# Kernel tuning notes

Measured on AMD Instinct MI355X. Metric: run time of the kernel, lower is better.

The kernel has to match this reference:

```python
import jax, jax.numpy as jnp
from jax import lax
import numpy as np

DN = ('NCHW', 'OIHW', 'NCHW')

def conv(x, w, b, stride=1, groups=1):
    y = lax.conv_general_dilated(x, w, (stride, stride), 'SAME',
                                 feature_group_count=groups, dimension_numbers=DN)
    return y + b[None, :, None, None]

def sep_conv(x, dw, pw, pb):
    # depthwise 3x3 -> pointwise 1x1 -> ReLU (BN is frozen at identity)
    y = lax.conv_general_dilated(x, dw, (1, 1), 'SAME',
                                 feature_group_count=x.shape[1], dimension_numbers=DN)
    return jax.nn.relu(conv(y, pw, pb))

def up2(x):
    return jnp.repeat(jnp.repeat(x, 2, axis=2), 2, axis=3)

def down2(x):
    return lax.reduce_window(x, -jnp.inf, lax.max, (1, 1, 2, 2), (1, 1, 2, 2), 'VALID')

def fuse(w, *xs):
    # fast normalized fusion
    w = jax.nn.relu(w)
    w = w / (jnp.sum(w) + 1e-4)
    out = w[0] * xs[0]
    for i in range(1, len(xs)):
        out = out + w[i] * xs[i]
    return out

def bifpn_layer(ps, dw, pw, pb, fw2, fw3):
    p3, p4, p5, p6, p7 = ps
    p6t = sep_conv(fuse(fw2[0], p6, up2(p7)),  dw[0], pw[0], pb[0])
    p5t = sep_conv(fuse(fw2[1], p5, up2(p6t)), dw[1], pw[1], pb[1])
    p4t = sep_conv(fuse(fw2[2], p4, up2(p5t)), dw[2], pw[2], pb[2])
    p3o = sep_conv(fuse(fw2[3], p3, up2(p4t)), dw[3], pw[3], pb[3])
    p4o = sep_conv(fuse(fw3[0], p4, p4t, down2(p3o)), dw[4], pw[4], pb[4])
    p5o = sep_conv(fuse(fw3[1], p5, p5t, down2(p4o)), dw[5], pw[5], pb[5])
    p6o = sep_conv(fuse(fw3[2], p6, p6t, down2(p5o)), dw[6], pw[6], pb[6])
    p7o = sep_conv(fuse(fw2[4], p7, down2(p6o)),      dw[7], pw[7], pb[7])
    return [p3o, p4o, p5o, p6o, p7o]

def make_anchors(img_size):
    # RetinaNet-style anchors: pyramid levels 3..7, 3 scales x 3 ratios
    ratios = np.array([0.5, 1.0, 2.0])
    scales = 2.0 ** (np.arange(3) / 3.0)
    boxes_all = []
    for lvl in range(3, 8):
        stride = 2 ** lvl
        size = 2 ** (lvl + 2)
        fs = img_size // stride
        ws = (size * scales[None, :] / np.sqrt(ratios)[:, None]).reshape(-1)  # [9]
        hs = (size * scales[None, :] * np.sqrt(ratios)[:, None]).reshape(-1)
        ctr = (np.arange(fs) + 0.5) * stride
        gy, gx = np.meshgrid(ctr, ctr, indexing='ij')
        centers = np.stack([gx, gy], -1).reshape(-1, 1, 2)      # [HW,1,2] (x,y)
        wh = np.stack([ws, hs], -1)[None]                       # [1,9,2]
        boxes = np.concatenate([centers - wh / 2, centers + wh / 2], -1).reshape(-1, 4)
        boxes_all.append(boxes)
    return jnp.asarray(np.concatenate(boxes_all, 0), jnp.float32)

def run_head(p, tw, tb, ow, ob, out_ch):
    x = p
    for i in range(tw.shape[0]):
        x = jax.nn.relu(conv(x, tw[i], tb[i]))
    y = conv(x, ow, ob)                                  # [B, 9*out_ch, H, W]
    B, _, H, W = y.shape
    return y.transpose(0, 2, 3, 1).reshape(B, H * W * 9, out_ch)

def setup_inputs() -> dict:
    key = jax.random.key(0)
    ks = iter(jax.random.split(key, 64))
    B, W, NC, ST, D = 4, 88, 90, 3, 4
    chans = [40, 80, 112, 192, 320]
    hw = [64, 32, 16, 8, 4]
    inp = {}
    for i, (c, h) in enumerate(zip(chans, hw)):
        inp[f'c{i+3}'] = jax.random.normal(next(ks), (B, c, h, h), jnp.float32)
        inp[f'lat_w{i+3}'] = jax.random.normal(next(ks), (W, c, 1, 1), jnp.float32) * 0.05
        inp[f'lat_b{i+3}'] = jnp.zeros((W,), jnp.float32)
    inp['bif_dw'] = jax.random.normal(next(ks), (ST, 8, W, 1, 3, 3), jnp.float32) * 0.1
    inp['bif_pw'] = jax.random.normal(next(ks), (ST, 8, W, W, 1, 1), jnp.float32) * 0.05
    inp['bif_pb'] = jnp.zeros((ST, 8, W), jnp.float32)
    inp['bif_fw2'] = jnp.ones((ST, 5, 2), jnp.float32)
    inp['bif_fw3'] = jnp.ones((ST, 3, 3), jnp.float32)
    inp['reg_tw'] = jax.random.normal(next(ks), (D, W, W, 3, 3), jnp.float32) * 0.03
    inp['reg_tb'] = jnp.zeros((D, W), jnp.float32)
    inp['reg_ow'] = jax.random.normal(next(ks), (36, W, 3, 3), jnp.float32) * 0.01
    inp['reg_ob'] = jnp.zeros((36,), jnp.float32)
    inp['cls_tw'] = jax.random.normal(next(ks), (D, W, W, 3, 3), jnp.float32) * 0.03
    inp['cls_tb'] = jnp.zeros((D, W), jnp.float32)
    inp['cls_ow'] = jax.random.normal(next(ks), (9 * NC, W, 3, 3), jnp.float32) * 0.01
    inp['cls_ob'] = jnp.full((9 * NC,), -np.log((1.0 - 0.01) / 0.01), jnp.float32)
    inp['img_size'] = 512
    return inp

def reference(c3, c4, c5, c6, c7,
              lat_w3, lat_b3, lat_w4, lat_b4, lat_w5, lat_b5,
              lat_w6, lat_b6, lat_w7, lat_b7,
              bif_dw, bif_pw, bif_pb, bif_fw2, bif_fw3,
              reg_tw, reg_tb, reg_ow, reg_ob,
              cls_tw, cls_tb, cls_ow, cls_ob,
              img_size):
    num_classes = cls_ow.shape[0] // 9
    ps = [conv(c3, lat_w3, lat_b3), conv(c4, lat_w4, lat_b4), conv(c5, lat_w5, lat_b5),
          conv(c6, lat_w6, lat_b6), conv(c7, lat_w7, lat_b7)]
    for s in range(bif_dw.shape[0]):
        ps = bifpn_layer(ps, bif_dw[s], bif_pw[s], bif_pb[s], bif_fw2[s], bif_fw3[s])
    regression = jnp.concatenate([run_head(p, reg_tw, reg_tb, reg_ow, reg_ob, 4) for p in ps], axis=1)
    classification = jnp.concatenate(
        [jax.nn.sigmoid(run_head(p, cls_tw, cls_tb, cls_ow, cls_ob, num_classes)) for p in ps], axis=1)
    anchors = make_anchors(int(img_size))
    return classification, regression, anchors
```

## Files before the change

kernel.cpp:

```cpp
#include <hip/hip_runtime.h>
#include <math.h>

#define TPB 256
static inline int cdiv(int a, int b) { return (a + b - 1) / b; }

typedef __attribute__((ext_vector_type(8))) short short8;
typedef __attribute__((ext_vector_type(4))) float floatx4;

__device__ __forceinline__ float bf2f(ushort u) {
    union { unsigned int u; float f; } v; v.u = ((unsigned int)u) << 16; return v.f;
}
__device__ __forceinline__ ushort f2bf(float f) {
    union { float f; unsigned int u; } v; v.f = f;
    unsigned int r = (v.u + 0x7FFFu + ((v.u >> 16) & 1u)) >> 16;
    return (ushort)r;
}

#define CONC_ROWS 21824
__device__ __forceinline__ void lvl_of(int row, int& lvl, int& base) {
    lvl = 0; base = 0;
    if (row >= 16384) { lvl = 1; base = 16384; }
    if (row >= 20480) { lvl = 2; base = 20480; }
    if (row >= 21504) { lvl = 3; base = 21504; }
    if (row >= 21760) { lvl = 4; base = 21760; }
}
__constant__ int LOFFc[5] = {0, 36864, 46080, 48384, 48960};

#define BSLAB 9216

__device__ __forceinline__ void gld_lds16(const ushort* g, ushort* l) {
    __builtin_amdgcn_global_load_lds(
        (const __attribute__((address_space(1))) unsigned int*)g,
        (__attribute__((address_space(3))) unsigned int*)l, 16, 0, 0);
}

__global__ void pack3_k(const float* __restrict__ w, ushort* __restrict__ Bp,
                        int Ntot, int CO, int total) {
    int idx = blockIdx.x * blockDim.x + threadIdx.x;
    if (idx >= total) return;
    int j = idx & 7; int t = idx >> 3;
    int n = t % Ntot; t /= Ntot;
    int g = t & 3; t >>= 2;
    int ks = t % 3; int tap = t / 3;
    int ci = ks * 32 + g * 8 + j;
    float v = (ci < 88 && n < CO) ? w[((size_t)n * 88 + ci) * 9 + tap] : 0.f;
    Bp[idx] = f2bf(v);
}

__global__ void pack_cls_k(const float* __restrict__ w, ushort* __restrict__ Bp) {
    int idx = blockIdx.x * blockDim.x + threadIdx.x;
    if (idx >= 746496) return;
    int j = idx & 7; int t = idx >> 3;
    int n = t % 96; t /= 96;
    int g = t & 3; t >>= 2;
    int ks = t % 3; t /= 3;
    int tap = t % 9; int nb = t / 9;
    int ci = ks * 32 + g * 8 + j;
    int co = nb * 96 + n;
    float v = (ci < 88 && co < 810) ? w[((size_t)co * 88 + ci) * 9 + tap] : 0.f;
    Bp[idx] = f2bf(v);
}

__global__ void pack_tw8_k(const float* __restrict__ rw, const float* __restrict__ cw,
                           ushort* __restrict__ Bp) {
    int idx = blockIdx.x * blockDim.x + threadIdx.x;
    if (idx >= 8 * 82944) return;
    int i = idx / 82944; int r = idx - i * 82944;
    const float* w = (i < 4) ? rw + (size_t)i * 69696 : cw + (size_t)(i - 4) * 69696;
    int j = r & 7; int t = r >> 3;
    int n = t % 96; t /= 96;
    int g = t & 3; t >>= 2;
    int ks = t % 3; int tap = t / 3;
    int ci = ks * 32 + g * 8 + j;
    float v = (ci < 88 && n < 88) ? w[((size_t)n * 88 + ci) * 9 + tap] : 0.f;
    Bp[idx] = f2bf(v);
}

__global__ void pack_pw_all_k(const float* __restrict__ pw, ushort* __restrict__ Bp,
                              int total) {
    int idx = blockIdx.x * blockDim.x + threadIdx.x;
    if (idx >= total) return;
    int cid = idx / BSLAB; int r = idx - cid * BSLAB;
    int j = r & 7; int t = r >> 3;
    int n = t % 96; t /= 96;
    int g = t & 3; int ks = t >> 2;
    int ci = ks * 32 + g * 8 + j;
    float v = (ci < 88 && n < 88) ? pw[(size_t)cid * 7744 + n * 88 + ci] : 0.f;
    Bp[idx] = f2bf(v);
}

__global__ void pack_lat_k(const float* __restrict__ w3, const float* __restrict__ w4,
                           const float* __restrict__ w5, const float* __restrict__ w6,
                           const float* __restrict__ w7, ushort* __restrict__ Bp) {
    int idx = blockIdx.x * blockDim.x + threadIdx.x;
    if (idx >= 76800) return;
    int l, off;
    if (idx < 6144)       { l = 0; off = 0; }
    else if (idx < 15360) { l = 1; off = 6144; }
    else if (idx < 27648) { l = 2; off = 15360; }
    else if (idx < 46080) { l = 3; off = 27648; }
    else                  { l = 4; off = 46080; }
    const float* w = l == 0 ? w3 : l == 1 ? w4 : l == 2 ? w5 : l == 3 ? w6 : w7;
    const int cins[5] = {40, 80, 112, 192, 320};
    int Cin = cins[l];
    int r = idx - off;
    int j = r & 7; int t = r >> 3;
    int n = t % 96; t /= 96;
    int g = t & 3; int ks = t >> 2;
    int ci = ks * 32 + g * 8 + j;
    float v = (ci < Cin && n < 88) ? w[(size_t)n * Cin + ci] : 0.f;
    Bp[idx] = f2bf(v);
}

__global__ __launch_bounds__(256)
void lateral_mfma_k(const float* __restrict__ x, const ushort* __restrict__ Bp,
                    const float* __restrict__ bias, ushort* __restrict__ out,
                    int Cin, int KS, int logHH) {
    __shared__ ushort As[64 * 40];
    int tid = threadIdx.x;
    int m0 = blockIdx.x * 64;
    int lane = tid & 63, l15 = lane & 15, g = (lane >> 4) & 3;
    int wave = tid >> 6, wm = wave & 1, wn = wave >> 1;
    floatx4 acc[2][3];
#pragma unroll
    for (int a = 0; a < 2; ++a)
#pragma unroll
        for (int b = 0; b < 3; ++b) acc[a][b] = (floatx4){0.f, 0.f, 0.f, 0.f};
    const short8* Bq = (const short8*)Bp;

    int p = m0 + lane;
    int n = p >> logHH, pp = p & ((1 << logHH) - 1);
    const float* xp = x + (((size_t)n * Cin) << logHH) + pp;

    for (int ks = 0; ks < KS; ++ks) {
        __syncthreads();
#pragma unroll
        for (int it = 0; it < 8; ++it) {
            int ciL = (tid >> 6) + it * 4;
            int ci = ks * 32 + ciL;
            float v = (ci < Cin) ? xp[(size_t)ci << logHH] : 0.f;
            As[lane * 40 + ciL] = f2bf(v);
        }
        __syncthreads();
        short8 a0 = *(const short8*)(&As[(wm * 32 + l15) * 40 + g * 8]);
        short8 a1 = *(const short8*)(&As[(wm * 32 + 16 + l15) * 40 + g * 8]);
        int bbase = (ks * 4 + g) * 96 + wn * 48 + l15;
#pragma unroll
        for (int nf = 0; nf < 3; ++nf) {
            short8 b = Bq[bbase + nf * 16];
            acc[0][nf] = __builtin_amdgcn_mfma_f32_16x16x32_bf16(a0, b, acc[0][nf], 0, 0, 0);
            acc[1][nf] = __builtin_amdgcn_mfma_f32_16x16x32_bf16(a1, b, acc[1][nf], 0, 0, 0);
        }
    }
    float bc[3];
#pragma unroll
    for (int nf = 0; nf < 3; ++nf) {
        int c = wn * 48 + nf * 16 + l15;
        bc[nf] = (c < 88) ? bias[c] : 0.f;
    }
#pragma unroll
    for (int mf = 0; mf < 2; ++mf)
#pragma unroll
        for (int r = 0; r < 4; ++r) {
            int pl = m0 + wm * 32 + mf * 16 + g * 4 + r;
#pragma unroll
            for (int nf = 0; nf < 3; ++nf) {
                int c = wn * 48 + nf * 16 + l15;
                out[(size_t)pl * 96 + c] = f2bf(acc[mf][nf][r] + bc[nf]);
            }
        }
}

template <int MODE>
__global__ __launch_bounds__(256, 2)
void sepconv_k(const ushort* __restrict__ a, const ushort* __restrict__ bsrc,
               const ushort* __restrict__ csrc, const float* __restrict__ fw,
               const float* __restrict__ dww, const ushort* __restrict__ Bp,
               const float* __restrict__ pbias, ushort* __restrict__ out,
               int logW) {
    __shared__ ushort Fs[195 * 104];
    __shared__ ushort Ds[64 * 104];
    __shared__ ushort Dwb[108 * 8];
    int tid = threadIdx.x;
    int W = 1 << logW, HH = W * W, log2HH = 2 * logW;
    int Mlv = 4 * HH;
    int HB = W + 1;
    int RS = 64 + 2 * HB;
    int pl0 = blockIdx.x * 64;
    float w0 = fmaxf(fw[0], 0.f), w1 = fmaxf(fw[1], 0.f);
    float w2 = (MODE == 2) ? fmaxf(fw[2], 0.f) : 0.f;
    float inv = 1.f / (w0 + w1 + w2 + 1e-4f);
    float w0i = w0 * inv, w1i = w1 * inv, w2i = w2 * inv;

    if (tid < 13) *(uint4*)(&Fs[194 * 104 + tid * 8]) = (uint4){0u, 0u, 0u, 0u};
    for (int i = tid; i < 108; i += 256) {
        int cg = i / 9, tap = i - cg * 9;
        ushort tmp[8];
#pragma unroll
        for (int j = 0; j < 8; ++j) {
            int c = cg * 8 + j;
            tmp[j] = (c < 88) ? f2bf(dww[c * 9 + tap]) : (ushort)0;
        }
        *(uint4*)(&Dwb[i * 8]) = *(uint4*)tmp;
    }
    for (int i = tid; i < RS * 12; i += 256) {
        int row = i / 12, cg = i - row * 12;
        int pl = pl0 - HB + row;
        uint4 res = {0u, 0u, 0u, 0u};
        if (pl >= 0 && pl < Mlv) {
            int n = pl >> log2HH, pp = pl & (HH - 1);
            int y = pp >> logW, x = pp & (W - 1);
            uint4 av = *(const uint4*)(a + (size_t)pl * 96 + cg * 8);
            const ushort* au = (const ushort*)&av;
            float f[8];
            if (MODE == 0) {
                int Wh = W >> 1;
                int bp = (n << (log2HH - 2)) + (y >> 1) * Wh + (x >> 1);
                uint4 bv = *(const uint4*)(bsrc + (size_t)bp * 96 + cg * 8);
                const ushort* bu = (const ushort*)&bv;
#pragma unroll
                for (int j = 0; j < 8; ++j)
                    f[j] = w0i * bf2f(au[j]) + w1i * bf2f(bu[j]);
            } else {
                int W2 = W << 1;
                const ushort* q = (MODE == 1 ? bsrc : csrc) +
                    ((size_t)((n << (log2HH + 2)) + (2 * y) * W2 + 2 * x)) * 96 + cg * 8;
                uint4 q0 = *(const uint4*)(q);
                uint4 q1 = *(const uint4*)(q + 96);
                uint4 q2 = *(const uint4*)(q + (size_t)W2 * 96);
                uint4 q3 = *(const uint4*)(q + (size_t)W2 * 96 + 96);
                const ushort* u0 = (const ushort*)&q0; const ushort* u1 = (const ushort*)&q1;
                const ushort* u2 = (const ushort*)&q2; const ushort* u3 = (const ushort*)&q3;
                if (MODE == 1) {
#pragma unroll
                    for (int j = 0; j < 8; ++j) {
                        float m = fmaxf(fmaxf(bf2f(u0[j]), bf2f(u1[j])),
                                        fmaxf(bf2f(u2[j]), bf2f(u3[j])));
                        f[j] = w0i * bf2f(au[j]) + w1i * m;
                    }
                } else {
                    uint4 b2v = *(const uint4*)(bsrc + (size_t)pl * 96 + cg * 8);
                    const ushort* b2u = (const ushort*)&b2v;
#pragma unroll
                    for (int j = 0; j < 8; ++j) {
                        float m = fmaxf(fmaxf(bf2f(u0[j]), bf2f(u1[j])),
                                        fmaxf(bf2f(u2[j]), bf2f(u3[j])));
                        f[j] = w0i * bf2f(au[j]) + w1i * bf2f(b2u[j]) + w2i * m;
                    }
                }
            }
            ushort tmp[8];
#pragma unroll
            for (int j = 0; j < 8; ++j) tmp[j] = f2bf(f[j]);
            res = *(uint4*)tmp;
        }
        *(uint4*)(&Fs[row * 104 + cg * 8]) = res;
    }
    __syncthreads();
    for (int i = tid; i < 768; i += 256) {
        int row = i / 12, cg = i - row * 12;
        int pl = pl0 + row;
        int pp = pl & (HH - 1);
        int y = pp >> logW, x = pp & (W - 1);
        float acc8[8] = {0.f, 0.f, 0.f, 0.f, 0.f, 0.f, 0.f, 0.f};
        if (cg < 11) {
#pragma unroll
            for (int tap = 0; tap < 9; ++tap) {
                int dy = tap / 3 - 1, dx = tap % 3 - 1;
                int sy = y + dy, sx = x + dx;
                bool pred = ((unsigned)sy < (unsigned)W) && ((unsigned)sx < (unsigned)W);
                int rsel = pred ? (row + HB + dy * W + dx) : 194;
                short8 fv = *(const short8*)(&Fs[rsel * 104 + cg * 8]);
                short8 wv = *(const short8*)(&Dwb[(cg * 9 + tap) * 8]);
#pragma unroll
                for (int j = 0; j < 8; ++j)
                    acc8[j] = fmaf(bf2f((ushort)fv[j]), bf2f((ushort)wv[j]), acc8[j]);
            }
        }
        ushort tmp[8];
#pragma unroll
        for (int j = 0; j < 8; ++j) tmp[j] = f2bf(acc8[j]);
        *(uint4*)(&Ds[row * 104 + cg * 8]) = *(uint4*)tmp;
    }
    __syncthreads();
    int lane = tid & 63, l15 = lane & 15, g = (lane >> 4) & 3;
    int wave = tid >> 6, wm = wave & 1, wn = wave >> 1;
    floatx4 acc[2][3];
#pragma unroll
    for (int aa = 0; aa < 2; ++aa)
#pragma unroll
        for (int bb = 0; bb < 3; ++bb) acc[aa][bb] = (floatx4){0.f, 0.f, 0.f, 0.f};
    const short8* Bq = (const short8*)Bp;
#pragma unroll
    for (int ks = 0; ks < 3; ++ks) {
        int k = ks * 32 + g * 8;
        short8 a0 = *(const short8*)(&Ds[(wm * 32 + l15) * 104 + k]);
        short8 a1 = *(const short8*)(&Ds[(wm * 32 + 16 + l15) * 104 + k]);
        int bbase = (ks * 4 + g) * 96 + wn * 48 + l15;
#pragma unroll
        for (int nf = 0; nf < 3; ++nf) {
            short8 b = Bq[bbase + nf * 16];
            acc[0][nf] = __builtin_amdgcn_mfma_f32_16x16x32_bf16(a0, b, acc[0][nf], 0, 0, 0);
            acc[1][nf] = __builtin_amdgcn_mfma_f32_16x16x32_bf16(a1, b, acc[1][nf], 0, 0, 0);
        }
    }
    float bc[3];
#pragma unroll
    for (int nf = 0; nf < 3; ++nf) {
        int c = wn * 48 + nf * 16 + l15;
        bc[nf] = (c < 88) ? pbias[c] : 0.f;
    }
#pragma unroll
    for (int mf = 0; mf < 2; ++mf)
#pragma unroll
        for (int r = 0; r < 4; ++r) {
            int pl = pl0 + wm * 32 + mf * 16 + g * 4 + r;
#pragma unroll
            for (int nf = 0; nf < 3; ++nf) {
                int c = wn * 48 + nf * 16 + l15;
                out[(size_t)pl * 96 + c] = f2bf(fmaxf(acc[mf][nf][r] + bc[nf], 0.f));
            }
        }
}

__global__ __launch_bounds__(256)
void tower_pipe_k(const ushort* __restrict__ inR, const ushort* __restrict__ inC,
                  const ushort* __restrict__ BpR, const ushort* __restrict__ BpC,
                  const float* __restrict__ bR, const float* __restrict__ bC,
                  ushort* __restrict__ outR, ushort* __restrict__ outC,
                  const ushort* __restrict__ zb) {
    __shared__ __align__(16) ushort Bs[2][BSLAB];
    int head = blockIdx.y;
    const ushort* in = head ? inC : inR;
    const ushort* Bg = head ? BpC : BpR;
    const float* bias = head ? bC : bR;
    ushort* out = head ? outC : outR;
    int tid = threadIdx.x;
    int m0 = blockIdx.x * 64;
    int lvl, base; lvl_of(m0, lvl, base);
    int logW = 6 - lvl, W = 1 << logW, HH = W * W;
    int pl0 = m0 - base;
    int lane = tid & 63, l15 = lane & 15, g = (lane >> 4) & 3;
    int wave = tid >> 6, wm = wave & 1, wn = wave >> 1;
    int ym[2], xm[2];
    const ushort* pbase[2];
#pragma unroll
    for (int mf = 0; mf < 2; ++mf) {
        int pl = pl0 + wm * 32 + mf * 16 + l15;
        int pp = pl & (HH - 1);
        ym[mf] = pp >> logW; xm[mf] = pp & (W - 1);
        pbase[mf] = in + (size_t)(base + pl) * 96 + g * 8;
    }
    const ushort* zbg = zb + g * 8;
    int fragoff = (g * 96 + wn * 48 + l15) * 8;

    auto stage = [&](int tap) {
        const ushort* src = Bg + tap * BSLAB;
        ushort* dst = (ushort*)Bs[tap & 1];
#pragma unroll
        for (int it = 0; it < 5; ++it) {
            int c = tid + it * 256;
            if (c < 1152) gld_lds16(src + (size_t)c * 8, dst + (size_t)c * 8);
        }
    };

    floatx4 acc[2][3];
#pragma unroll
    for (int aa = 0; aa < 2; ++aa)
#pragma unroll
        for (int bb = 0; bb < 3; ++bb) acc[aa][bb] = (floatx4){0.f, 0.f, 0.f, 0.f};

    stage(0);
    __syncthreads();
#pragma unroll
    for (int tap = 0; tap < 9; ++tap) {
        if (tap < 8) stage(tap + 1);
        const ushort* Bb = (const ushort*)Bs[tap & 1];
        const int dy = tap / 3 - 1, dx = tap % 3 - 1;
        int off96 = (dy * W + dx) * 96;
        const ushort* ap[2];
#pragma unroll
        for (int mf = 0; mf < 2; ++mf) {
            bool pred = ((unsigned)(ym[mf] + dy) < (unsigned)W) &&
                        ((unsigned)(xm[mf] + dx) < (unsigned)W);
            ap[mf] = pred ? (pbase[mf] + off96) : zbg;
        }
#pragma unroll
        for (int ks = 0; ks < 3; ++ks) {
            short8 a0 = *(const short8*)(ap[0] + ks * 32);
            short8 a1 = *(const short8*)(ap[1] + ks * 32);
            const ushort* bb = Bb + ks * 3072 + fragoff;
#pragma unroll
            for (int nf = 0; nf < 3; ++nf) {
                short8 b = *(const short8*)(bb + nf * 128);
                acc[0][nf] = __builtin_amdgcn_mfma_f32_16x16x32_bf16(a0, b, acc[0][nf], 0, 0, 0);
                acc[1][nf] = __builtin_amdgcn_mfma_f32_16x16x32_bf16(a1, b, acc[1][nf], 0, 0, 0);
            }
        }
        __syncthreads();
    }
    float bc[3];
#pragma unroll
    for (int nf = 0; nf < 3; ++nf) {
        int c = wn * 48 + nf * 16 + l15;
        bc[nf] = (c < 88) ? bias[c] : 0.f;
    }
#pragma unroll
    for (int mf = 0; mf < 2; ++mf)
#pragma unroll
        for (int r = 0; r < 4; ++r) {
            int pl = pl0 + wm * 32 + mf * 16 + g * 4 + r;
#pragma unroll
            for (int nf = 0; nf < 3; ++nf) {
                int c = wn * 48 + nf * 16 + l15;
                out[(size_t)(base + pl) * 96 + c] = f2bf(fmaxf(acc[mf][nf][r] + bc[nf], 0.f));
            }
        }
}

__global__ __launch_bounds__(256)
void heads_pipe_k(const ushort* __restrict__ xr, const ushort* __restrict__ xc,
                  const ushort* __restrict__ BpR, const ushort* __restrict__ BpC,
                  const float* __restrict__ bR, const float* __restrict__ bC,
                  float* __restrict__ outR, float* __restrict__ outC,
                  const ushort* __restrict__ zb) {
    __shared__ __align__(16) ushort Bs[2][BSLAB];
    int yb = blockIdx.y;
    bool isReg = (yb == 0);
    const ushort* in = isReg ? xr : xc;
    const ushort* Bg = isReg ? BpR : (BpC + (size_t)(yb - 1) * 9 * BSLAB);
    const float* bias = isReg ? bR : bC;
    float* outb = isReg ? outR : outC;
    const int C9 = isReg ? 36 : 810;
    const int OC = isReg ? 4 : 90;
    const int n0b = isReg ? 0 : (yb - 1) * 96;

    int tid = threadIdx.x;
    int m0 = blockIdx.x * 64;
    int lvl, base; lvl_of(m0, lvl, base);
    int logW = 6 - lvl, W = 1 << logW, HH = W * W, log2HH = 2 * logW;
    int pl0 = m0 - base;
    int lane = tid & 63, l15 = lane & 15, g = (lane >> 4) & 3;
    int wave = tid >> 6, wm = wave & 1, wn = wave >> 1;
    int ym[2], xm[2];
    const ushort* pbase[2];
#pragma unroll
    for (int mf = 0; mf < 2; ++mf) {
        int pl = pl0 + wm * 32 + mf * 16 + l15;
        int pp = pl & (HH - 1);
        ym[mf] = pp >> logW; xm[mf] = pp & (W - 1);
        pbase[mf] = in + (size_t)(base + pl) * 96 + g * 8;
    }
    const ushort* zbg = zb + g * 8;
    int fragoff = (g * 96 + wn * 48 + l15) * 8;

    auto stage = [&](int tap) {
        const ushort* src = Bg + tap * BSLAB;
        ushort* dst = (ushort*)Bs[tap & 1];
#pragma unroll
        for (int it = 0; it < 5; ++it) {
            int c = tid + it * 256;
            if (c < 1152) gld_lds16(src + (size_t)c * 8, dst + (size_t)c * 8);
        }
    };

    floatx4 acc[2][3];
#pragma unroll
    for (int aa = 0; aa < 2; ++aa)
#pragma unroll
        for (int bb = 0; bb < 3; ++bb) acc[aa][bb] = (floatx4){0.f, 0.f, 0.f, 0.f};

    stage(0);
    __syncthreads();
#pragma unroll
    for (int tap = 0; tap < 9; ++tap) {
        if (tap < 8) stage(tap + 1);
        const ushort* Bb = (const ushort*)Bs[tap & 1];
        const int dy = tap / 3 - 1, dx = tap % 3 - 1;
        int off96 = (dy * W + dx) * 96;
        const ushort* ap[2];
#pragma unroll
        for (int mf = 0; mf < 2; ++mf) {
            bool pred = ((unsigned)(ym[mf] + dy) < (unsigned)W) &&
                        ((unsigned)(xm[mf] + dx) < (unsigned)W);
            ap[mf] = pred ? (pbase[mf] + off96) : zbg;
        }
#pragma unroll
        for (int ks = 0; ks < 3; ++ks) {
            short8 a0 = *(const short8*)(ap[0] + ks * 32);
            short8 a1 = *(const short8*)(ap[1] + ks * 32);
            const ushort* bb = Bb + ks * 3072 + fragoff;
#pragma unroll
            for (int nf = 0; nf < 3; ++nf) {
                short8 b = *(const short8*)(bb + nf * 128);
                acc[0][nf] = __builtin_amdgcn_mfma_f32_16x16x32_bf16(a0, b, acc[0][nf], 0, 0, 0);
                acc[1][nf] = __builtin_amdgcn_mfma_f32_16x16x32_bf16(a1, b, acc[1][nf], 0, 0, 0);
            }
        }
        __syncthreads();
    }
#pragma unroll
    for (int nf = 0; nf < 3; ++nf) {
        int c = n0b + wn * 48 + nf * 16 + l15;
        if (c >= C9) continue;
        float bcv = bias[c];
        int a = c / OC, kk = c - a * OC;
#pragma unroll
        for (int mf = 0; mf < 2; ++mf)
#pragma unroll
            for (int r = 0; r < 4; ++r) {
                int pl = pl0 + wm * 32 + mf * 16 + g * 4 + r;
                int n = pl >> log2HH, pp = pl & (HH - 1);
                float v = acc[mf][nf][r] + bcv;
                if (!isReg) v = 1.f / (1.f + expf(-v));
                outb[((size_t)n * 49104 + LOFFc[lvl] + (size_t)pp * 9 + a) * OC + kk] = v;
            }
    }
}

__global__ void anchors_k(float* __restrict__ out, ushort* __restrict__ zb) {
    int idx = blockIdx.x * blockDim.x + threadIdx.x;
    if (idx < 48) ((unsigned int*)zb)[idx] = 0u;
    if (idx >= 49104) return;
    const int offs[6] = {0, 36864, 46080, 48384, 48960, 49104};
    int l = 0;
    while (idx >= offs[l + 1]) ++l;
    int j = idx - offs[l];
    int a = j % 9;
    int p = j / 9;
    int fs = 64 >> l;
    int stride = 8 << l;
    float size = (float)(32 << l);
    int ix = p % fs, iy = p / fs;
    float cx = (ix + 0.5f) * (float)stride;
    float cy = (iy + 0.5f) * (float)stride;
    const float scl[3] = {1.0f, 1.2599210498948732f, 1.5874010519681994f};
    const float sqr[3] = {0.7071067811865476f, 1.0f, 1.4142135623730951f};
    int r = a / 3, s = a % 3;
    float w = size * scl[s] / sqr[r];
    float h = size * scl[s] * sqr[r];
    float* o = out + (size_t)idx * 4;
    o[0] = cx - 0.5f * w;
    o[1] = cy - 0.5f * h;
    o[2] = cx + 0.5f * w;
    o[3] = cy + 0.5f * h;
}


extern "C" void kernel_launch(void* const* d_in, const int* in_sizes, int n_in,
                              void* d_out, int out_size, void* d_ws, size_t ws_size,
                              hipStream_t stream) {
    const float* c_in[5]  = {(const float*)d_in[0],  (const float*)d_in[3],
                             (const float*)d_in[6],  (const float*)d_in[9],
                             (const float*)d_in[12]};
    const float* lat_w[5] = {(const float*)d_in[1],  (const float*)d_in[4],
                             (const float*)d_in[7],  (const float*)d_in[10],
                             (const float*)d_in[13]};
    const float* lat_b[5] = {(const float*)d_in[2],  (const float*)d_in[5],
                             (const float*)d_in[8],  (const float*)d_in[11],
                             (const float*)d_in[14]};
    const float* bif_dw  = (const float*)d_in[15];
    const float* bif_pw  = (const float*)d_in[16];
    const float* bif_pb  = (const float*)d_in[17];
    const float* bif_fw2 = (const float*)d_in[18];
    const float* bif_fw3 = (const float*)d_in[19];
    const float* reg_tw  = (const float*)d_in[20];
    const float* reg_tb  = (const float*)d_in[21];
    const float* reg_ow  = (const float*)d_in[22];
    const float* reg_ob  = (const float*)d_in[23];
    const float* cls_tw  = (const float*)d_in[24];
    const float* cls_tb  = (const float*)d_in[25];
    const float* cls_ow  = (const float*)d_in[26];
    const float* cls_ob  = (const float*)d_in[27];

    const int CINL[5] = {40, 80, 112, 192, 320};
    const int KSL[5]  = {2, 3, 4, 6, 10};
    const int LATO[5] = {0, 6144, 15360, 27648, 46080};
    const int ROFF[5] = {0, 16384, 20480, 21504, 21760};
    const int ML[5]   = {16384, 4096, 1024, 256, 64};
    const size_t CONC = (size_t)CONC_ROWS * 96;

    ushort* ws = (ushort*)d_ws;
    size_t off = 0;
    ushort* CA = ws + off; off += CONC;
    ushort* CB = ws + off; off += CONC;
    ushort* T4 = ws + off; off += (size_t)4096 * 96;
    ushort* T5 = ws + off; off += (size_t)1024 * 96;
    ushort* T6 = ws + off; off += (size_t)256 * 96;
    ushort* HXR0 = ws + off; off += CONC;
    ushort* HXR1 = ws + off; off += CONC;
    ushort* HXC0 = ws + off; off += CONC;
    ushort* HXC1 = ws + off; off += CONC;
    ushort* BP_PW  = ws + off; off += (size_t)24 * BSLAB;
    ushort* BP_TW  = ws + off; off += (size_t)8 * 82944;
    ushort* BP_RO  = ws + off; off += (size_t)82944;
    ushort* BP_CO  = ws + off; off += (size_t)746496;
    ushort* BP_LAT = ws + off; off += (size_t)76800;
    ushort* ZB     = ws + off; off += 96;
    (void)ws_size; (void)n_in; (void)in_sizes; (void)out_size;

    pack_pw_all_k<<<cdiv(24 * BSLAB, TPB), TPB, 0, stream>>>(bif_pw, BP_PW, 24 * BSLAB);
    pack_tw8_k<<<cdiv(8 * 82944, TPB), TPB, 0, stream>>>(reg_tw, cls_tw, BP_TW);
    pack3_k<<<cdiv(82944, TPB), TPB, 0, stream>>>(reg_ow, BP_RO, 96, 36, 82944);
    pack_cls_k<<<cdiv(746496, TPB), TPB, 0, stream>>>(cls_ow, BP_CO);
    pack_lat_k<<<cdiv(76800, TPB), TPB, 0, stream>>>(
        lat_w[0], lat_w[1], lat_w[2], lat_w[3], lat_w[4], BP_LAT);

    float* cls_base = (float*)d_out;
    float* reg_base = cls_base + (size_t)4 * 49104 * 90;
    float* anc_base = reg_base + (size_t)4 * 49104 * 4;
    anchors_k<<<cdiv(49104, TPB), TPB, 0, stream>>>(anc_base, ZB);

    for (int l = 0; l < 5; ++l) {
        int logHH = 2 * (6 - l);
        lateral_mfma_k<<<ML[l] / 64, 256, 0, stream>>>(
            c_in[l], BP_LAT + LATO[l], lat_b[l], CA + (size_t)ROFF[l] * 96,
            CINL[l], KSL[l], logHH);
    }

    ushort* cur = CA; ushort* nxt = CB;
    for (int s = 0; s < 3; ++s) {
        const float* dws = bif_dw + (size_t)s * 8 * 792;
        const float* pbs = bif_pb + (size_t)s * 8 * 88;
        const float* f2  = bif_fw2 + (size_t)s * 10;
        const float* f3  = bif_fw3 + (size_t)s * 9;
        auto LP = [&](ushort* buf, int l) { return buf + (size_t)ROFF[l] * 96; };
        auto BPW = [&](int ci) { return BP_PW + (size_t)(s * 8 + ci) * BSLAB; };

        sepconv_k<0><<<ML[3] / 64, 256, 0, stream>>>(
            LP(cur, 3), LP(cur, 4), nullptr, f2 + 0, dws + 0 * 792, BPW(0), pbs + 0 * 88, T6, 3);
        sepconv_k<0><<<ML[2] / 64, 256, 0, stream>>>(
            LP(cur, 2), T6, nullptr, f2 + 2, dws + 1 * 792, BPW(1), pbs + 1 * 88, T5, 4);
        sepconv_k<0><<<ML[1] / 64, 256, 0, stream>>>(
            LP(cur, 1), T5, nullptr, f2 + 4, dws + 2 * 792, BPW(2), pbs + 2 * 88, T4, 5);
        sepconv_k<0><<<ML[0] / 64, 256, 0, stream>>>(
            LP(cur, 0), T4, nullptr, f2 + 6, dws + 3 * 792, BPW(3), pbs + 3 * 88, LP(nxt, 0), 6);
        sepconv_k<2><<<ML[1] / 64, 256, 0, stream>>>(
            LP(cur, 1), T4, LP(nxt, 0), f3 + 0, dws + 4 * 792, BPW(4), pbs + 4 * 88, LP(nxt, 1), 5);
        sepconv_k<2><<<ML[2] / 64, 256, 0, stream>>>(
            LP(cur, 2), T5, LP(nxt, 1), f3 + 3, dws + 5 * 792, BPW(5), pbs + 5 * 88, LP(nxt, 2), 4);
        sepconv_k<2><<<ML[3] / 64, 256, 0, stream>>>(
            LP(cur, 3), T6, LP(nxt, 2), f3 + 6, dws + 6 * 792, BPW(6), pbs + 6 * 88, LP(nxt, 3), 3);
        sepconv_k<1><<<ML[4] / 64, 256, 0, stream>>>(
            LP(cur, 4), LP(nxt, 3), nullptr, f2 + 8, dws + 7 * 792, BPW(7), pbs + 7 * 88, LP(nxt, 4), 2);

        ushort* tp = cur; cur = nxt; nxt = tp;
    }

    const int GB = CONC_ROWS / 64;
    ushort* hxr[2] = {HXR0, HXR1};
    ushort* hxc[2] = {HXC0, HXC1};
    const ushort* xr = cur;
    const ushort* xc = cur;
    for (int i = 0; i < 4; ++i) {
        tower_pipe_k<<<dim3(GB, 2), 256, 0, stream>>>(
            xr, xc, BP_TW + (size_t)i * 82944, BP_TW + (size_t)(4 + i) * 82944,
            reg_tb + i * 88, cls_tb + i * 88, hxr[i & 1], hxc[i & 1], ZB);
        xr = hxr[i & 1]; xc = hxc[i & 1];
    }
    heads_pipe_k<<<dim3(GB, 10), 256, 0, stream>>>(
        xr, xc, BP_RO, BP_CO, reg_ob, cls_ob, reg_base, cls_base, ZB);
}
```

Measured before the change: 647.9 us.

## Fuse lateral convs and BiFPN layers into one persistent kernel with grid barriers

Result: slower. 1.688 ms (+160.6%).

```diff
diff --git a/kernel.cpp b/kernel.cpp
--- a/kernel.cpp
+++ b/kernel.cpp
@@ -34,91 +34,94 @@
         (__attribute__((address_space(3))) unsigned int*)l, 16, 0, 0);
 }
 
-__global__ void pack3_k(const float* __restrict__ w, ushort* __restrict__ Bp,
-                        int Ntot, int CO, int total) {
-    int idx = blockIdx.x * blockDim.x + threadIdx.x;
-    if (idx >= total) return;
-    int j = idx & 7; int t = idx >> 3;
-    int n = t % Ntot; t /= Ntot;
-    int g = t & 3; t >>= 2;
-    int ks = t % 3; int tap = t / 3;
-    int ci = ks * 32 + g * 8 + j;
-    float v = (ci < 88 && n < CO) ? w[((size_t)n * 88 + ci) * 9 + tap] : 0.f;
-    Bp[idx] = f2bf(v);
-}
-
-__global__ void pack_cls_k(const float* __restrict__ w, ushort* __restrict__ Bp) {
-    int idx = blockIdx.x * blockDim.x + threadIdx.x;
-    if (idx >= 746496) return;
-    int j = idx & 7; int t = idx >> 3;
-    int n = t % 96; t /= 96;
-    int g = t & 3; t >>= 2;
-    int ks = t % 3; t /= 3;
-    int tap = t % 9; int nb = t / 9;
-    int ci = ks * 32 + g * 8 + j;
-    int co = nb * 96 + n;
-    float v = (ci < 88 && co < 810) ? w[((size_t)co * 88 + ci) * 9 + tap] : 0.f;
-    Bp[idx] = f2bf(v);
-}
-
-__global__ void pack_tw8_k(const float* __restrict__ rw, const float* __restrict__ cw,
-                           ushort* __restrict__ Bp) {
-    int idx = blockIdx.x * blockDim.x + threadIdx.x;
-    if (idx >= 8 * 82944) return;
-    int i = idx / 82944; int r = idx - i * 82944;
-    const float* w = (i < 4) ? rw + (size_t)i * 69696 : cw + (size_t)(i - 4) * 69696;
-    int j = r & 7; int t = r >> 3;
-    int n = t % 96; t /= 96;
-    int g = t & 3; t >>= 2;
-    int ks = t % 3; int tap = t / 3;
-    int ci = ks * 32 + g * 8 + j;
-    float v = (ci < 88 && n < 88) ? w[((size_t)n * 88 + ci) * 9 + tap] : 0.f;
-    Bp[idx] = f2bf(v);
-}
-
-__global__ void pack_pw_all_k(const float* __restrict__ pw, ushort* __restrict__ Bp,
-                              int total) {
-    int idx = blockIdx.x * blockDim.x + threadIdx.x;
-    if (idx >= total) return;
-    int cid = idx / BSLAB; int r = idx - cid * BSLAB;
-    int j = r & 7; int t = r >> 3;
-    int n = t % 96; t /= 96;
-    int g = t & 3; int ks = t >> 2;
-    int ci = ks * 32 + g * 8 + j;
-    float v = (ci < 88 && n < 88) ? pw[(size_t)cid * 7744 + n * 88 + ci] : 0.f;
-    Bp[idx] = f2bf(v);
-}
-
-__global__ void pack_lat_k(const float* __restrict__ w3, const float* __restrict__ w4,
+__global__ void pack_all_k(const float* __restrict__ pw, const float* __restrict__ rw,
+                           const float* __restrict__ cw, const float* __restrict__ row_,
+                           const float* __restrict__ cow,
+                           const float* __restrict__ w3, const float* __restrict__ w4,
                            const float* __restrict__ w5, const float* __restrict__ w6,
-                           const float* __restrict__ w7, ushort* __restrict__ Bp) {
-    int idx = blockIdx.x * blockDim.x + threadIdx.x;
-    if (idx >= 76800) return;
-    int l, off;
-    if (idx < 6144)       { l = 0; off = 0; }
-    else if (idx < 15360) { l = 1; off = 6144; }
-    else if (idx < 27648) { l = 2; off = 15360; }
-    else if (idx < 46080) { l = 3; off = 27648; }
-    else                  { l = 4; off = 46080; }
-    const float* w = l == 0 ? w3 : l == 1 ? w4 : l == 2 ? w5 : l == 3 ? w6 : w7;
-    const int cins[5] = {40, 80, 112, 192, 320};
-    int Cin = cins[l];
-    int r = idx - off;
-    int j = r & 7; int t = r >> 3;
-    int n = t % 96; t /= 96;
-    int g = t & 3; int ks = t >> 2;
-    int ci = ks * 32 + g * 8 + j;
-    float v = (ci < Cin && n < 88) ? w[(size_t)n * Cin + ci] : 0.f;
-    Bp[idx] = f2bf(v);
-}
-
-__global__ __launch_bounds__(256)
-void lateral_mfma_k(const float* __restrict__ x, const ushort* __restrict__ Bp,
-                    const float* __restrict__ bias, ushort* __restrict__ out,
-                    int Cin, int KS, int logHH) {
-    __shared__ ushort As[64 * 40];
+                           const float* __restrict__ w7,
+                           ushort* __restrict__ BP_PW, ushort* __restrict__ BP_TW,
+                           ushort* __restrict__ BP_RO, ushort* __restrict__ BP_CO,
+                           ushort* __restrict__ BP_LAT) {
+    int gid = blockIdx.x * blockDim.x + threadIdx.x;
+    if (gid < 221184) {
+        int idx = gid;
+        int cid = idx / BSLAB; int r = idx - cid * BSLAB;
+        int j = r & 7; int t = r >> 3;
+        int n = t % 96; t /= 96;
+        int g = t & 3; int ks = t >> 2;
+        int ci = ks * 32 + g * 8 + j;
+        float v = (ci < 88 && n < 88) ? pw[(size_t)cid * 7744 + n * 88 + ci] : 0.f;
+        BP_PW[idx] = f2bf(v);
+    } else if (gid < 884736) {
+        int idx = gid - 221184;
+        int i = idx / 82944; int r = idx - i * 82944;
+        const float* w = (i < 4) ? rw + (size_t)i * 69696 : cw + (size_t)(i - 4) * 69696;
+        int j = r & 7; int t = r >> 3;
+        int n = t % 96; t /= 96;
+        int g = t & 3; t >>= 2;
+        int ks = t % 3; int tap = t / 3;
+        int ci = ks * 32 + g * 8 + j;
+        float v = (ci < 88 && n < 88) ? w[((size_t)n * 88 + ci) * 9 + tap] : 0.f;
+        BP_TW[idx] = f2bf(v);
+    } else if (gid < 967680) {
+        int idx = gid - 884736;
+        int j = idx & 7; int t = idx >> 3;
+        int n = t % 96; t /= 96;
+        int g = t & 3; t >>= 2;
+        int ks = t % 3; int tap = t / 3;
+        int ci = ks * 32 + g * 8 + j;
+        float v = (ci < 88 && n < 36) ? row_[((size_t)n * 88 + ci) * 9 + tap] : 0.f;
+        BP_RO[idx] = f2bf(v);
+    } else if (gid < 1714176) {
+        int idx = gid - 967680;
+        int j = idx & 7; int t = idx >> 3;
+        int n = t % 96; t /= 96;
+        int g = t & 3; t >>= 2;
+        int ks = t % 3; t /= 3;
+        int tap = t % 9; int nb = t / 9;
+        int ci = ks * 32 + g * 8 + j;
+        int co = nb * 96 + n;
+        float v = (ci < 88 && co < 810) ? cow[((size_t)co * 88 + ci) * 9 + tap] : 0.f;
+        BP_CO[idx] = f2bf(v);
+    } else if (gid < 1790976) {
+        int idx = gid - 1714176;
+        int l, off;
+        if (idx < 6144)       { l = 0; off = 0; }
+        else if (idx < 15360) { l = 1; off = 6144; }
+        else if (idx < 27648) { l = 2; off = 15360; }
+        else if (idx < 46080) { l = 3; off = 27648; }
+        else                  { l = 4; off = 46080; }
+        const float* w = l == 0 ? w3 : l == 1 ? w4 : l == 2 ? w5 : l == 3 ? w6 : w7;
+        const int cins[5] = {40, 80, 112, 192, 320};
+        int Cin = cins[l];
+        int r = idx - off;
+        int j = r & 7; int t = r >> 3;
+        int n = t % 96; t /= 96;
+        int g = t & 3; int ks = t >> 2;
+        int ci = ks * 32 + g * 8 + j;
+        float v = (ci < Cin && n < 88) ? w[(size_t)n * Cin + ci] : 0.f;
+        BP_LAT[idx] = f2bf(v);
+    }
+}
+
+__device__ __forceinline__ void gbar(int* cnt, int target) {
+    __syncthreads();
+    if (threadIdx.x == 0) {
+        __threadfence();
+        __hip_atomic_fetch_add(cnt, 1, __ATOMIC_RELEASE, __HIP_MEMORY_SCOPE_AGENT);
+        while (__hip_atomic_load(cnt, __ATOMIC_ACQUIRE, __HIP_MEMORY_SCOPE_AGENT) < target)
+            __builtin_amdgcn_s_sleep(2);
+        __threadfence();
+    }
+    __syncthreads();
+}
+
+__device__ void lateral_work(const float* __restrict__ x, const ushort* __restrict__ Bp,
+                             const float* __restrict__ bias, ushort* __restrict__ out,
+                             int Cin, int KS, int logHH, int blk, ushort* As) {
     int tid = threadIdx.x;
-    int m0 = blockIdx.x * 64;
+    int m0 = blk * 64;
     int lane = tid & 63, l15 = lane & 15, g = (lane >> 4) & 3;
     int wave = tid >> 6, wm = wave & 1, wn = wave >> 1;
     floatx4 acc[2][3];
@@ -171,24 +174,20 @@
         }
 }
 
-template <int MODE>
-__global__ __launch_bounds__(256, 2)
-void sepconv_k(const ushort* __restrict__ a, const ushort* __restrict__ bsrc,
-               const ushort* __restrict__ csrc, const float* __restrict__ fw,
-               const float* __restrict__ dww, const ushort* __restrict__ Bp,
-               const float* __restrict__ pbias, ushort* __restrict__ out,
-               int logW) {
-    __shared__ ushort Fs[195 * 104];
-    __shared__ ushort Ds[64 * 104];
-    __shared__ ushort Dwb[108 * 8];
+__device__ void sepconv_work(int mode, const ushort* __restrict__ a,
+                             const ushort* __restrict__ bsrc, const ushort* __restrict__ csrc,
+                             const float* __restrict__ fw, const float* __restrict__ dww,
+                             const ushort* __restrict__ Bp, const float* __restrict__ pbias,
+                             ushort* __restrict__ out, int logW, int blk,
+                             ushort* Fs, ushort* Ds, ushort* Dwb) {
     int tid = threadIdx.x;
     int W = 1 << logW, HH = W * W, log2HH = 2 * logW;
     int Mlv = 4 * HH;
     int HB = W + 1;
     int RS = 64 + 2 * HB;
-    int pl0 = blockIdx.x * 64;
+    int pl0 = blk * 64;
     float w0 = fmaxf(fw[0], 0.f), w1 = fmaxf(fw[1], 0.f);
-    float w2 = (MODE == 2) ? fmaxf(fw[2], 0.f) : 0.f;
+    float w2 = (mode == 2) ? fmaxf(fw[2], 0.f) : 0.f;
     float inv = 1.f / (w0 + w1 + w2 + 1e-4f);
     float w0i = w0 * inv, w1i = w1 * inv, w2i = w2 * inv;
 
@@ -213,7 +212,7 @@
             uint4 av = *(const uint4*)(a + (size_t)pl * 96 + cg * 8);
             const ushort* au = (const ushort*)&av;
             float f[8];
-            if (MODE == 0) {
+            if (mode == 0) {
                 int Wh = W >> 1;
                 int bp = (n << (log2HH - 2)) + (y >> 1) * Wh + (x >> 1);
                 uint4 bv = *(const uint4*)(bsrc + (size_t)bp * 96 + cg * 8);
@@ -223,7 +222,7 @@
                     f[j] = w0i * bf2f(au[j]) + w1i * bf2f(bu[j]);
             } else {
                 int W2 = W << 1;
-                const ushort* q = (MODE == 1 ? bsrc : csrc) +
+                const ushort* q = (mode == 1 ? bsrc : csrc) +
                     ((size_t)((n << (log2HH + 2)) + (2 * y) * W2 + 2 * x)) * 96 + cg * 8;
                 uint4 q0 = *(const uint4*)(q);
                 uint4 q1 = *(const uint4*)(q + 96);
@@ -231,7 +230,7 @@
                 uint4 q3 = *(const uint4*)(q + (size_t)W2 * 96 + 96);
                 const ushort* u0 = (const ushort*)&q0; const ushort* u1 = (const ushort*)&q1;
                 const ushort* u2 = (const ushort*)&q2; const ushort* u3 = (const ushort*)&q3;
-                if (MODE == 1) {
+                if (mode == 1) {
 #pragma unroll
                     for (int j = 0; j < 8; ++j) {
                         float m = fmaxf(fmaxf(bf2f(u0[j]), bf2f(u1[j])),
@@ -321,6 +320,83 @@
                 out[(size_t)pl * 96 + c] = f2bf(fmaxf(acc[mf][nf][r] + bc[nf], 0.f));
             }
         }
+}
+
+__global__ __launch_bounds__(256)
+void bifpn_mega_k(const float* __restrict__ c3, const float* __restrict__ c4,
+                  const float* __restrict__ c5, const float* __restrict__ c6,
+                  const float* __restrict__ c7,
+                  const float* __restrict__ lb3, const float* __restrict__ lb4,
+                  const float* __restrict__ lb5, const float* __restrict__ lb6,
+                  const float* __restrict__ lb7,
+                  const ushort* __restrict__ BP_LAT,
+                  const float* __restrict__ bif_dw, const float* __restrict__ bif_pb,
+                  const float* __restrict__ bif_fw2, const float* __restrict__ bif_fw3,
+                  const ushort* __restrict__ BP_PW,
+                  ushort* __restrict__ CA, ushort* __restrict__ CB,
+                  ushort* __restrict__ T4, ushort* __restrict__ T5, ushort* __restrict__ T6,
+                  int* __restrict__ cnt) {
+    __shared__ ushort Fs[195 * 104];
+    __shared__ ushort Ds[64 * 104];
+    __shared__ ushort Dwb[108 * 8];
+    const int NB = gridDim.x;
+    int bi = 0;
+
+    {
+        const float* xs[5] = {c3, c4, c5, c6, c7};
+        const float* bs[5] = {lb3, lb4, lb5, lb6, lb7};
+        const int CINL[5] = {40, 80, 112, 192, 320};
+        const int KSL[5]  = {2, 3, 4, 6, 10};
+        const int LATO[5] = {0, 6144, 15360, 27648, 46080};
+        const int WOFF[6] = {0, 256, 320, 336, 340, 341};
+        const int ROFF[5] = {0, 16384, 20480, 21504, 21760};
+        for (int w = blockIdx.x; w < 341; w += NB) {
+            int l = 0;
+            while (w >= WOFF[l + 1]) ++l;
+            int blk = w - WOFF[l];
+            lateral_work(xs[l], BP_LAT + LATO[l], bs[l], CA + (size_t)ROFF[l] * 96,
+                         CINL[l], KSL[l], 2 * (6 - l), blk, Fs );
+        }
+    }
+    gbar(&cnt[bi++], NB);
+
+    ushort* cur = CA; ushort* nxt = CB;
+    const int ROFF[5] = {0, 16384, 20480, 21504, 21760};
+    for (int s = 0; s < 3; ++s) {
+        const float* dws = bif_dw + (size_t)s * 8 * 792;
+        const float* pbs = bif_pb + (size_t)s * 8 * 88;
+        const float* f2  = bif_fw2 + (size_t)s * 10;
+        const float* f3  = bif_fw3 + (size_t)s * 9;
+        const ushort* PW = BP_PW + (size_t)s * 8 * BSLAB;
+        int bx = blockIdx.x;
+
+        if (bx < 4) sepconv_work(0, cur + (size_t)ROFF[3]*96, cur + (size_t)ROFF[4]*96, nullptr,
+                                 f2 + 0, dws + 0*792, PW + 0*BSLAB, pbs + 0*88, T6, 3, bx, Fs, Ds, Dwb);
+        gbar(&cnt[bi++], NB);
+        if (bx < 16) sepconv_work(0, cur + (size_t)ROFF[2]*96, T6, nullptr,
+                                  f2 + 2, dws + 1*792, PW + 1*BSLAB, pbs + 1*88, T5, 4, bx, Fs, Ds, Dwb);
+        gbar(&cnt[bi++], NB);
+        if (bx < 64) sepconv_work(0, cur + (size_t)ROFF[1]*96, T5, nullptr,
+                                  f2 + 4, dws + 2*792, PW + 2*BSLAB, pbs + 2*88, T4, 5, bx, Fs, Ds, Dwb);
+        gbar(&cnt[bi++], NB);
+        sepconv_work(0, cur + (size_t)ROFF[0]*96, T4, nullptr,
+                     f2 + 6, dws + 3*792, PW + 3*BSLAB, pbs + 3*88, nxt + (size_t)ROFF[0]*96, 6, bx, Fs, Ds, Dwb);
+        gbar(&cnt[bi++], NB);
+        if (bx < 64) sepconv_work(2, cur + (size_t)ROFF[1]*96, T4, nxt + (size_t)ROFF[0]*96,
+                                  f3 + 0, dws + 4*792, PW + 4*BSLAB, pbs + 4*88, nxt + (size_t)ROFF[1]*96, 5, bx, Fs, Ds, Dwb);
+        gbar(&cnt[bi++], NB);
+        if (bx < 16) sepconv_work(2, cur + (size_t)ROFF[2]*96, T5, nxt + (size_t)ROFF[1]*96,
+                                  f3 + 3, dws + 5*792, PW + 5*BSLAB, pbs + 5*88, nxt + (size_t)ROFF[2]*96, 4, bx, Fs, Ds, Dwb);
+        gbar(&cnt[bi++], NB);
+        if (bx < 4) sepconv_work(2, cur + (size_t)ROFF[3]*96, T6, nxt + (size_t)ROFF[2]*96,
+                                 f3 + 6, dws + 6*792, PW + 6*BSLAB, pbs + 6*88, nxt + (size_t)ROFF[3]*96, 3, bx, Fs, Ds, Dwb);
+        gbar(&cnt[bi++], NB);
+        if (bx < 1) sepconv_work(1, cur + (size_t)ROFF[4]*96, nxt + (size_t)ROFF[3]*96, nullptr,
+                                 f2 + 8, dws + 7*792, PW + 7*BSLAB, pbs + 7*88, nxt + (size_t)ROFF[4]*96, 2, bx, Fs, Ds, Dwb);
+        gbar(&cnt[bi++], NB);
+
+        ushort* tp = cur; cur = nxt; nxt = tp;
+    }
 }
 
 __global__ __launch_bounds__(256)
@@ -573,14 +649,10 @@
     const float* cls_ow  = (const float*)d_in[26];
     const float* cls_ob  = (const float*)d_in[27];
 
-    const int CINL[5] = {40, 80, 112, 192, 320};
-    const int KSL[5]  = {2, 3, 4, 6, 10};
-    const int LATO[5] = {0, 6144, 15360, 27648, 46080};
-    const int ROFF[5] = {0, 16384, 20480, 21504, 21760};
-    const int ML[5]   = {16384, 4096, 1024, 256, 64};
     const size_t CONC = (size_t)CONC_ROWS * 96;
 
-    ushort* ws = (ushort*)d_ws;
+    int* CNT = (int*)d_ws;
+    ushort* ws = (ushort*)d_ws + 64;
     size_t off = 0;
     ushort* CA = ws + off; off += CONC;
     ushort* CB = ws + off; off += CONC;
@@ -599,53 +671,24 @@
     ushort* ZB     = ws + off; off += 96;
     (void)ws_size; (void)n_in; (void)in_sizes; (void)out_size;
 
-    pack_pw_all_k<<<cdiv(24 * BSLAB, TPB), TPB, 0, stream>>>(bif_pw, BP_PW, 24 * BSLAB);
-    pack_tw8_k<<<cdiv(8 * 82944, TPB), TPB, 0, stream>>>(reg_tw, cls_tw, BP_TW);
-    pack3_k<<<cdiv(82944, TPB), TPB, 0, stream>>>(reg_ow, BP_RO, 96, 36, 82944);
-    pack_cls_k<<<cdiv(746496, TPB), TPB, 0, stream>>>(cls_ow, BP_CO);
-    pack_lat_k<<<cdiv(76800, TPB), TPB, 0, stream>>>(
-        lat_w[0], lat_w[1], lat_w[2], lat_w[3], lat_w[4], BP_LAT);
+    hipMemsetAsync(d_ws, 0, 128, stream);
+
+    pack_all_k<<<cdiv(1790976, TPB), TPB, 0, stream>>>(
+        bif_pw, reg_tw, cls_tw, reg_ow, cls_ow,
+        lat_w[0], lat_w[1], lat_w[2], lat_w[3], lat_w[4],
+        BP_PW, BP_TW, BP_RO, BP_CO, BP_LAT);
 
     float* cls_base = (float*)d_out;
     float* reg_base = cls_base + (size_t)4 * 49104 * 90;
     float* anc_base = reg_base + (size_t)4 * 49104 * 4;
     anchors_k<<<cdiv(49104, TPB), TPB, 0, stream>>>(anc_base, ZB);
 
-    for (int l = 0; l < 5; ++l) {
-        int logHH = 2 * (6 - l);
-        lateral_mfma_k<<<ML[l] / 64, 256, 0, stream>>>(
-            c_in[l], BP_LAT + LATO[l], lat_b[l], CA + (size_t)ROFF[l] * 96,
-            CINL[l], KSL[l], logHH);
-    }
-
-    ushort* cur = CA; ushort* nxt = CB;
-    for (int s = 0; s < 3; ++s) {
-        const float* dws = bif_dw + (size_t)s * 8 * 792;
-        const float* pbs = bif_pb + (size_t)s * 8 * 88;
-        const float* f2  = bif_fw2 + (size_t)s * 10;
-        const float* f3  = bif_fw3 + (size_t)s * 9;
-        auto LP = [&](ushort* buf, int l) { return buf + (size_t)ROFF[l] * 96; };
-        auto BPW = [&](int ci) { return BP_PW + (size_t)(s * 8 + ci) * BSLAB; };
-
-        sepconv_k<0><<<ML[3] / 64, 256, 0, stream>>>(
-            LP(cur, 3), LP(cur, 4), nullptr, f2 + 0, dws + 0 * 792, BPW(0), pbs + 0 * 88, T6, 3);
-        sepconv_k<0><<<ML[2] / 64, 256, 0, stream>>>(
-            LP(cur, 2), T6, nullptr, f2 + 2, dws + 1 * 792, BPW(1), pbs + 1 * 88, T5, 4);
-        sepconv_k<0><<<ML[1] / 64, 256, 0, stream>>>(
-            LP(cur, 1), T5, nullptr, f2 + 4, dws + 2 * 792, BPW(2), pbs + 2 * 88, T4, 5);
-        sepconv_k<0><<<ML[0] / 64, 256, 0, stream>>>(
-            LP(cur, 0), T4, nullptr, f2 + 6, dws + 3 * 792, BPW(3), pbs + 3 * 88, LP(nxt, 0), 6);
-        sepconv_k<2><<<ML[1] / 64, 256, 0, stream>>>(
-            LP(cur, 1), T4, LP(nxt, 0), f3 + 0, dws + 4 * 792, BPW(4), pbs + 4 * 88, LP(nxt, 1), 5);
-        sepconv_k<2><<<ML[2] / 64, 256, 0, stream>>>(
-            LP(cur, 2), T5, LP(nxt, 1), f3 + 3, dws + 5 * 792, BPW(5), pbs + 5 * 88, LP(nxt, 2), 4);
-        sepconv_k<2><<<ML[3] / 64, 256, 0, stream>>>(
-            LP(cur, 3), T6, LP(nxt, 2), f3 + 6, dws + 6 * 792, BPW(6), pbs + 6 * 88, LP(nxt, 3), 3);
-        sepconv_k<1><<<ML[4] / 64, 256, 0, stream>>>(
-            LP(cur, 4), LP(nxt, 3), nullptr, f2 + 8, dws + 7 * 792, BPW(7), pbs + 7 * 88, LP(nxt, 4), 2);
-
-        ushort* tp = cur; cur = nxt; nxt = tp;
-    }
+    bifpn_mega_k<<<256, 256, 0, stream>>>(
+        c_in[0], c_in[1], c_in[2], c_in[3], c_in[4],
+        lat_b[0], lat_b[1], lat_b[2], lat_b[3], lat_b[4],
+        BP_LAT, bif_dw, bif_pb, bif_fw2, bif_fw3, BP_PW,
+        CA, CB, T4, T5, T6, CNT);
+    ushort* cur = CB;
 
     const int GB = CONC_ROWS / 64;
     ushort* hxr[2] = {HXR0, HXR1};
```
